# Kernel tuning notes

Measured on AMD Instinct MI355X. Metric: run time of the kernel, lower is better.

## Reference

```python
import jax, jax.numpy as jnp
import numpy as np

B, T, V, Dw, Df, H, L, F_ = 16, 96, 32000, 512, 512, 1024, 100, 64
EPS = 1e-8
SOS = 0


def setup_inputs() -> dict:
    key = jax.random.key(0)
    ks = jax.random.split(key, 24)
    rn = lambda k, s, sc=0.02: (jax.random.normal(k, s) * sc).astype(jnp.float32)
    pos_mask = (jax.random.uniform(ks[1], (B, F_, L)) < 0.3).astype(jnp.float32)
    pos_mask = jnp.maximum(pos_mask, jax.nn.one_hot(jnp.zeros((B, F_), jnp.int32), L))
    return {
        "fact_embeddings": rn(ks[0], (B, F_, Df), 1.0),
        "pos_mask": pos_mask,
        "emb": rn(ks[2], (V, Dw), 0.05),
        "W_ih": rn(ks[3], (4 * H, Df + Dw + L)),
        "W_hh": rn(ks[4], (4 * H, H)),
        "b_ih": jnp.zeros(4 * H, jnp.float32),
        "b_hh": jnp.zeros(4 * H, jnp.float32),
        "Wf1": rn(ks[5], (H, H + Df)), "bf1": jnp.zeros(H, jnp.float32),
        "Wf2": rn(ks[6], (Df, H)), "bf2": jnp.zeros(Df, jnp.float32),
        "Wc1": rn(ks[7], (H, H + Df)), "bc1": jnp.zeros(H, jnp.float32),
        "Wc2": rn(ks[8], (1, H)), "bc2": jnp.zeros(1, jnp.float32),
        "Wv1": rn(ks[9], (H, H + Df)), "bv1": jnp.zeros(H, jnp.float32),
        "Wv2": rn(ks[10], (Dw, H)), "bv2": jnp.zeros(Dw, jnp.float32),
        "Wp1": rn(ks[11], (H, H + Df)), "bp1": jnp.zeros(H, jnp.float32),
        "Wp2": rn(ks[12], (100, H)), "bp2": jnp.zeros(100, jnp.float32),
        "WP": rn(ks[13], (L, 100)), "bP": jnp.zeros(L, jnp.float32),
        "true_w": jax.random.randint(ks[14], (B, T), 0, L),
        "true_a": jax.random.randint(ks[15], (B, T), 0, F_),
        "true_z": jax.random.randint(ks[16], (B, T), 0, 2),
        "num_facts": jax.random.randint(ks[17], (B,), 1, F_),
    }


def reference(fact_embeddings, pos_mask, emb, W_ih, W_hh, b_ih, b_hh,
              Wf1, bf1, Wf2, bf2, Wc1, bc1, Wc2, bc2,
              Wv1, bv1, Wv2, bv2, Wp1, bp1, Wp2, bp2, WP, bP,
              true_w, true_a, true_z, num_facts):
    def mlp(x, W1, b1, W2, b2):
        return W2 @ jax.nn.relu(W1 @ x + b1) + b2

    def single(fe, pmask_b, tw, ta, tz, nf):
        # fe: [F_, Df]  pmask_b: [F_, L]  tw/ta/tz: [T]
        idx = jnp.arange(F_)
        valid = (idx < nf).astype(jnp.float32)
        attn_mask = jnp.where(idx == F_ - 1, 1.0, valid)  # NaF slot always allowed
        e_k = (fe * valid[:, None]).sum(0) / nf.astype(jnp.float32)

        def step(carry, inputs):
            a_prev, h, c, wv, wo = carry
            w_t, a_true, z_true = inputs
            x = jnp.concatenate([a_prev, wv, wo])  # [Df+Dw+L]
            gates = W_ih @ x + b_ih + W_hh @ h + b_hh
            i_g, f_g, g_g, o_g = jnp.split(gates, 4)
            c = jax.nn.sigmoid(f_g) * c + jax.nn.sigmoid(i_g) * jnp.tanh(g_g)
            h = jax.nn.sigmoid(o_g) * jnp.tanh(c)
            oe = jnp.concatenate([h, e_k])
            k_fact = mlp(oe, Wf1, bf1, Wf2, bf2)           # [Df]
            prob_a = jax.nn.softmax(fe @ k_fact)           # [F_]
            m = attn_mask * prob_a + EPS
            m = m / m.sum()
            log_m = jnp.log(m)
            a_idx = jnp.argmax(m)
            a_vec = fe[a_idx]
            oa = jnp.concatenate([h, a_vec])
            z = jax.nn.sigmoid(mlp(oa, Wc1, bc1, Wc2, bc2))[0]
            k_voca = mlp(oa, Wv1, bv1, Wv2, bv2)           # [Dw]
            log_w = jax.nn.log_softmax(emb @ k_voca)       # [V]
            k_pos = mlp(oa, Wp1, bp1, Wp2, bp2)            # [100]
            prob_pos = jax.nn.softmax(WP @ k_pos + bP)     # [L]
            mp = pmask_b[a_true] * prob_pos + EPS
            mp = mp / mp.sum()
            log_pos = jnp.log(mp)
            zf = z_true.astype(jnp.float32)
            loss = (-log_m[a_true]
                    + jnp.where(z_true == 0, -log_w[w_t], -log_pos[w_t])
                    - (zf * jnp.log(z) + (1.0 - zf) * jnp.log(1.0 - z)))
            wv_next = jnp.where(z_true == 0, emb[w_t], jnp.zeros(Dw, jnp.float32))
            wo_next = jnp.where(z_true == 0, jnp.zeros(L, jnp.float32), jax.nn.one_hot(w_t, L))
            return (a_vec, h, c, wv_next, wo_next), loss

        carry0 = (jnp.zeros(Df, jnp.float32), jnp.zeros(H, jnp.float32),
                  jnp.zeros(H, jnp.float32), emb[SOS], jnp.zeros(L, jnp.float32))
        _, losses = jax.lax.scan(step, carry0, (tw, ta, tz))
        return losses.sum()

    return jax.vmap(single)(fact_embeddings, pos_mask, true_w, true_a, true_z, num_facts).sum()
```

## Files before the change

### kernel.cpp

```cpp
#include <hip/hip_runtime.h>
#include <math.h>

#define TT 96
#define VV 32000
#define EPSF 1e-8f

typedef __attribute__((ext_vector_type(8))) short short8;
typedef __attribute__((ext_vector_type(4))) float f4v;

__device__ __forceinline__ float wsum64(float v){
  #pragma unroll
  for (int m=32;m>0;m>>=1) v += __shfl_xor(v,m);
  return v;
}
__device__ __forceinline__ float sigm(float x){ return 1.0f/(1.0f+expf(-x)); }
__device__ __forceinline__ float softplus(float x){ return x>20.0f ? x : log1pf(expf(x)); }
__device__ __forceinline__ float bf2f(unsigned short u){ return __uint_as_float(((unsigned)u)<<16); }
__device__ __forceinline__ unsigned short f2bf(float f){
  unsigned u = __float_as_uint(f);
  return (unsigned short)((u + 0x7fffu + ((u>>16)&1u)) >> 16);
}

__device__ __forceinline__ void st_dc(float* p, float v){
  __hip_atomic_store(p, v, __ATOMIC_RELAXED, __HIP_MEMORY_SCOPE_AGENT);
}
__device__ __forceinline__ void st_dc_i(int* p, int v){
  __hip_atomic_store(p, v, __ATOMIC_RELAXED, __HIP_MEMORY_SCOPE_AGENT);
}
__device__ __forceinline__ int ld_dc_i(const int* p){
  return __hip_atomic_load(p, __ATOMIC_RELAXED, __HIP_MEMORY_SCOPE_AGENT);
}
__device__ __forceinline__ unsigned ld_cnt(const unsigned* p){
  return __hip_atomic_load(p, __ATOMIC_RELAXED, __HIP_MEMORY_SCOPE_AGENT);
}
__device__ __forceinline__ float2 ld_dc_2(const float* p){
  union { unsigned long long u; float2 f; } cv;
  cv.u = __hip_atomic_load((const unsigned long long*)p, __ATOMIC_RELAXED, __HIP_MEMORY_SCOPE_AGENT);
  return cv.f;
}

__device__ __forceinline__ void bar_full(unsigned* cntA, unsigned* rel, unsigned epoch){
  __syncthreads();
  if (threadIdx.x == 0)
    __hip_atomic_fetch_add(cntA + (blockIdx.x & 7)*64, 1u, __ATOMIC_RELAXED, __HIP_MEMORY_SCOPE_AGENT);
  if (blockIdx.x == 0){
    if (threadIdx.x < 64){
      unsigned tgt = epoch * 32u;
      while (true){
        unsigned v = (threadIdx.x < 8) ? ld_cnt(cntA + threadIdx.x*64) : tgt;
        if (__all(v >= tgt)) break;
        __builtin_amdgcn_s_sleep(1);
      }
      if (threadIdx.x == 0)
        __hip_atomic_store(rel, epoch, __ATOMIC_RELAXED, __HIP_MEMORY_SCOPE_AGENT);
    }
  } else {
    if (threadIdx.x == 0){
      while (ld_cnt(rel) < epoch) __builtin_amdgcn_s_sleep(1);
    }
  }
  __syncthreads();
}

__device__ __forceinline__ void core_chunk(
  const float4* __restrict__ w0, const float4* __restrict__ w1,
  const float4* __restrict__ w2, const float4* __restrict__ w3,
  const float4* __restrict__ xl, int l, int g, float (&acc)[4][4])
{
  #pragma unroll
  for (int kt=0; kt<8; kt++){
    int i = kt*16 + l;
    float4 a0=w0[i], a1=w1[i], a2=w2[i], a3=w3[i];
    #pragma unroll
    for (int j=0;j<4;j++){
      float4 x = xl[(4*g+j)*129 + i];
      acc[0][j] += a0.x*x.x + a0.y*x.y + a0.z*x.z + a0.w*x.w;
      acc[1][j] += a1.x*x.x + a1.y*x.y + a1.z*x.z + a1.w*x.w;
      acc[2][j] += a2.x*x.x + a2.y*x.y + a2.z*x.z + a2.w*x.w;
      acc[3][j] += a3.x*x.x + a3.y*x.y + a3.z*x.z + a3.w*x.w;
    }
  }
}

__device__ __forceinline__ float reduce_pick(float (&acc)[4][4], int l){
  float r = 0.f;
  #pragma unroll
  for (int ri=0;ri<4;ri++)
  #pragma unroll
  for (int j=0;j<4;j++){
    float v = acc[ri][j];
    v += __shfl_xor(v,1); v += __shfl_xor(v,2);
    v += __shfl_xor(v,4); v += __shfl_xor(v,8);
    if (l == ri*4+j) r = v;
  }
  return r;
}

__global__ __launch_bounds__(256) void k_phase1(
  const float* __restrict__ Whh, float* __restrict__ hall,
  const float* __restrict__ Pw, const float* __restrict__ Pa,
  int* __restrict__ aall, float* __restrict__ c,
  const float* __restrict__ Wf1, const float* __restrict__ cf,
  float* __restrict__ tf,
  const float* __restrict__ Gb, const float* __restrict__ gb0,
  const int* __restrict__ ta, const int* __restrict__ nfp,
  float* __restrict__ loss,
  unsigned* __restrict__ cntA, unsigned* __restrict__ cntB,
  unsigned* __restrict__ rel)
{
  __shared__ float4 xl[16*129];
  __shared__ float sg[256];
  __shared__ float sS[64];
  __shared__ int   sai[16];
  int tid = threadIdx.x, lane = tid & 63, wave = tid >> 6;
  int l = lane & 15, g = lane >> 4;
  int wg = blockIdx.x;

  for (int t=0; t<TT; t++){
    {
      int j0 = wg*4;
      const float4* h4 = (const float4*)hall + (size_t)t*4096;
      float acc[4][4] = {};
      for (int kc=0; kc<2; kc++){
        for (int idx=tid; idx<2048; idx+=256){
          int b = idx>>7, i = idx&127;
          xl[b*129+i] = h4[b*256 + kc*128 + i];
        }
        __syncthreads();
        const float4* w0 = (const float4*)(Whh + (size_t)(wave*1024 + j0+0)*1024) + kc*128;
        const float4* w1 = (const float4*)(Whh + (size_t)(wave*1024 + j0+1)*1024) + kc*128;
        const float4* w2 = (const float4*)(Whh + (size_t)(wave*1024 + j0+2)*1024) + kc*128;
        const float4* w3 = (const float4*)(Whh + (size_t)(wave*1024 + j0+3)*1024) + kc*128;
        core_chunk(w0,w1,w2,w3, xl, l, g, acc);
        __syncthreads();
      }
      float v = reduce_pick(acc, l);
      if (t > 0 && tid < 64){
        bool need = (tid < 16);
        while (true){
          int vv = need ? ld_dc_i(&aall[(t-1)*64 + tid]) : 1;
          if (__all(vv != 0)){ if (need) sai[tid] = vv - 1; break; }
          __builtin_amdgcn_s_sleep(1);
        }
      }
      __syncthreads();
      int r = l>>2;
      int b = g*4 + (l&3);
      int row = wave*1024 + j0 + r;
      float e = __builtin_nontemporal_load(Pw + ((size_t)(b*96+t))*4096 + row);
      if (t > 0){
        int ai = sai[b];
        e += __builtin_nontemporal_load(Pa + ((size_t)(b*64+ai))*4096 + row);
      }
      sg[wave*64 + r*16 + b] = v + e;
      __syncthreads();
      if (tid < 64){
        int jj = j0 + (tid>>4), bb = tid&15;
        float ig = sg[  0 + (tid>>4)*16 + bb];
        float fg = sg[ 64 + (tid>>4)*16 + bb];
        float gg = sg[128 + (tid>>4)*16 + bb];
        float og = sg[192 + (tid>>4)*16 + bb];
        int ci = bb*1024 + jj;
        float cn = sigm(fg)*c[ci] + sigm(ig)*tanhf(gg);
        c[ci] = cn;
        st_dc(&hall[((size_t)(t+1)*16 + bb)*1024 + jj], sigm(og)*tanhf(cn));
      }
    }
    bar_full(cntA, rel, (unsigned)(t+1));

    if (wg < 64){
      int rl0 = wg*16 + wave*4;
      const float4* h4 = (const float4*)hall + (size_t)(t+1)*4096;
      float acc[4][4] = {};
      for (int kc=0; kc<2; kc++){
        for (int idx=tid; idx<2048; idx+=256){
          int b = idx>>7, i = idx&127;
          xl[b*129+i] = h4[b*256 + kc*128 + i];
        }
        __syncthreads();
        const float4* w0 = (const float4*)(Wf1 + (size_t)(rl0+0)*1536) + kc*128;
        const float4* w1 = (const float4*)(Wf1 + (size_t)(rl0+1)*1536) + kc*128;
        const float4* w2 = (const float4*)(Wf1 + (size_t)(rl0+2)*1536) + kc*128;
        const float4* w3 = (const float4*)(Wf1 + (size_t)(rl0+3)*1536) + kc*128;
        core_chunk(w0,w1,w2,w3, xl, l, g, acc);
        __syncthreads();
      }
      float v = reduce_pick(acc, l);
      int rl = rl0 + (l>>2);
      int b = g*4 + (l&3);
      float* tfb = tf + (t&1)*16384;
      st_dc(&tfb[b*1024 + rl], fmaxf(v + cf[b*1024 + rl], 0.f));
      __syncthreads();
      if (tid == 0)
        __hip_atomic_fetch_add(cntB + (wg&7)*64, 1u, __ATOMIC_RELAXED, __HIP_MEMORY_SCOPE_AGENT);
    }

    if (wg >= 240){
      int b = wg - 240;
      if (tid < 64){
        unsigned tgt = (unsigned)(t+1) * 8u;
        while (true){
          unsigned vv = (tid < 8) ? ld_cnt(cntB + tid*64) : tgt;
          if (__all(vv >= tgt)) break;
          __builtin_amdgcn_s_sleep(1);
        }
      }
      __syncthreads();
      const float* tfb = tf + (t&1)*16384;
      float* stf = (float*)xl;
      {
        const float* src = tfb + b*1024;
        float2 c0 = ld_dc_2(src + 4*tid + 0);
        float2 c1 = ld_dc_2(src + 4*tid + 2);
        ((float2*)stf)[2*tid+0] = c0;
        ((float2*)stf)[2*tid+1] = c1;
      }
      __syncthreads();
      int f = tid>>2, q = tid&3;
      const float4* G4 = (const float4*)(Gb + (size_t)(b*64+f)*1024);
      const float4* st4 = (const float4*)stf;
      float acc = 0.f;
      for (int j=0;j<64;j++){
        int i = q*64 + j;
        float4 a = G4[i], x = st4[i];
        acc += a.x*x.x + a.y*x.y + a.z*x.z + a.w*x.w;
      }
      acc += __shfl_xor(acc,1);
      acc += __shfl_xor(acc,2);
      if (q==0) sS[f] = acc + gb0[b*64+f];
      __syncthreads();
      if (tid < 64){
        int nf = nfp[b];
        float s = sS[tid];
        float mx = s;
        #pragma unroll
        for (int m=32;m>0;m>>=1) mx = fmaxf(mx, __shfl_xor(mx,m));
        float p = expf(s - mx);
        float ps = wsum64(p);
        p /= ps;
        bool mask = (tid < nf) || (tid == 63);
        float mval = mask ? (p + EPSF) : EPSF;
        float msum = wsum64(mval);
        float bv = mval; int bi2 = tid;
        #pragma unroll
        for (int m=32;m>0;m>>=1){
          float ov = __shfl_xor(bv,m); int oi = __shfl_xor(bi2,m);
          if (ov > bv || (ov == bv && oi < bi2)){ bv = ov; bi2 = oi; }
        }
        int at = ta[b*TT + t];
        float mat = __shfl(mval, at);
        if (tid == 0){
          atomicAdd(loss, -(logf(mat) - logf(msum)));
          st_dc_i(&aall[t*64 + b], bi2 + 1);
        }
      }
      __syncthreads();
    }
  }
}


__global__ __launch_bounds__(256) void k2_cvp(
  const float* __restrict__ Wc1, const float* __restrict__ Wv1,
  const float* __restrict__ Wp1, const float* __restrict__ hall,
  const float* __restrict__ Ph, const int* __restrict__ aall,
  const float* __restrict__ bc1, const float* __restrict__ bv1,
  const float* __restrict__ bp1, float* __restrict__ tcvp)
{
  __shared__ float4 xl[16*129];
  int tid = threadIdx.x, lane = tid & 63, wave = tid >> 6;
  int l = lane & 15, g = lane >> 4;
  int seg = blockIdx.x >> 6;
  int rl0 = (blockIdx.x & 63)*16 + wave*4;
  const float* W = (seg==0)?Wc1:(seg==1)?Wv1:Wp1;
  const float4* h4 = (const float4*)hall + (size_t)(16 + blockIdx.y*16)*256;
  float acc[4][4] = {};
  for (int kc=0; kc<2; kc++){
    for (int idx=tid; idx<2048; idx+=256){
      int cc = idx>>7, i = idx&127;
      xl[cc*129+i] = h4[cc*256 + kc*128 + i];
    }
    __syncthreads();
    const float4* w0 = (const float4*)(W + (size_t)(rl0+0)*1536) + kc*128;
    const float4* w1 = (const float4*)(W + (size_t)(rl0+1)*1536) + kc*128;
    const float4* w2 = (const float4*)(W + (size_t)(rl0+2)*1536) + kc*128;
    const float4* w3 = (const float4*)(W + (size_t)(rl0+3)*1536) + kc*128;
    core_chunk(w0,w1,w2,w3, xl, l, g, acc);
    __syncthreads();
  }
  float v = reduce_pick(acc, l);
  int rl = rl0 + (l>>2);
  int n = blockIdx.y*16 + g*4 + (l&3);
  int b = n & 15;
  int ai = aall[(n>>4)*64 + (n&15)] - 1;
  const float* bias = (seg==0)?bc1:(seg==1)?bv1:bp1;
  float vv = v + Ph[((size_t)(b*64+ai))*3072 + seg*1024 + rl] + bias[rl];
  tcvp[(size_t)n*3072 + seg*1024 + rl] = fmaxf(vv, 0.f);
}

__global__ __launch_bounds__(256) void k2_heads2(
  const float* __restrict__ Wv2, const float* __restrict__ bv2,
  const float* __restrict__ Wp2, const float* __restrict__ bp2,
  const float* __restrict__ Wc2, const float* __restrict__ bc2,
  const float* __restrict__ tcvp, unsigned short* __restrict__ kvh,
  float* __restrict__ kpall, float* __restrict__ zlall)
{
  __shared__ float4 xl[16*129];
  int tid = threadIdx.x, lane = tid & 63, wave = tid >> 6;
  int l = lane & 15, g = lane >> 4;
  int bx = blockIdx.x;
  int seg = (bx < 32) ? 0 : (bx < 39) ? 1 : 2;
  int rb  = (seg==0) ? bx*16 : (seg==1) ? (bx-32)*16 : 0;
  int rl0 = rb + wave*4;
  const float* WS = (seg==0)?Wv2:(seg==1)?Wp2:Wc2;
  int maxr = (seg==0)?511:(seg==1)?99:0;
  int xoff4 = (seg==0)?256:(seg==1)?512:0;
  const float4* X4 = (const float4*)tcvp;
  float acc[4][4] = {};
  for (int kc=0; kc<2; kc++){
    for (int idx=tid; idx<2048; idx+=256){
      int cc = idx>>7, i = idx&127;
      xl[cc*129+i] = X4[(size_t)(blockIdx.y*16+cc)*768 + xoff4 + kc*128 + i];
    }
    __syncthreads();
    const float4* w0 = (const float4*)(WS + (size_t)min(rl0+0,maxr)*1024) + kc*128;
    const float4* w1 = (const float4*)(WS + (size_t)min(rl0+1,maxr)*1024) + kc*128;
    const float4* w2 = (const float4*)(WS + (size_t)min(rl0+2,maxr)*1024) + kc*128;
    const float4* w3 = (const float4*)(WS + (size_t)min(rl0+3,maxr)*1024) + kc*128;
    core_chunk(w0,w1,w2,w3, xl, l, g, acc);
    __syncthreads();
  }
  float v = reduce_pick(acc, l);
  int rl = rl0 + (l>>2);
  int n = blockIdx.y*16 + g*4 + (l&3);
  if (seg==0) kvh[(size_t)n*512 + rl] = f2bf(v + bv2[rl]);
  else if (seg==1){ if (rl < 100) kpall[n*128 + rl] = v + bp2[rl]; }
  else { if (rl == 0) zlall[n] = v + bc2[0]; }
}

__global__ __launch_bounds__(256) void k2_vocab(
  const unsigned short* __restrict__ embh, const unsigned short* __restrict__ kvh,
  float2* __restrict__ part)
{
  int wid = blockIdx.x*4 + (threadIdx.x>>6);
  int lane = threadIdx.x & 63;
  int mtile = wid % 500, ntile = wid / 500;
  int mrow = mtile*64 + (lane&15);
  int ncol = ntile*64 + (lane&15);
  int ko = (lane>>4)*8;
  f4v acc[4][4];
  #pragma unroll
  for (int i=0;i<4;i++)
  #pragma unroll
  for (int j=0;j<4;j++)
  #pragma unroll
  for (int r=0;r<4;r++) acc[i][j][r] = 0.f;
  for (int kk=0; kk<512; kk+=32){
    short8 af[4], bfr[4];
    #pragma unroll
    for (int i=0;i<4;i++)
      af[i] = *(const short8*)(embh + (size_t)(mrow+16*i)*512 + kk + ko);
    #pragma unroll
    for (int i=0;i<4;i++)
      bfr[i] = *(const short8*)(kvh + (size_t)(ncol+16*i)*512 + kk + ko);
    #pragma unroll
    for (int i=0;i<4;i++)
      #pragma unroll
      for (int j=0;j<4;j++)
        acc[i][j] = __builtin_amdgcn_mfma_f32_16x16x32_bf16(af[i], bfr[j], acc[i][j], 0,0,0);
  }
  int q = lane>>4;
  #pragma unroll
  for (int j=0;j<4;j++){
    float mx = -3.4e38f;
    #pragma unroll
    for (int i=0;i<4;i++)
    #pragma unroll
    for (int r=0;r<4;r++) mx = fmaxf(mx, acc[i][j][r]);
    mx = fmaxf(mx, __shfl_xor(mx,16));
    mx = fmaxf(mx, __shfl_xor(mx,32));
    float s = 0.f;
    #pragma unroll
    for (int i=0;i<4;i++)
    #pragma unroll
    for (int r=0;r<4;r++) s += expf(acc[i][j][r] - mx);
    s += __shfl_xor(s,16);
    s += __shfl_xor(s,32);
    if (q==0){
      int col = ntile*64 + 16*j + (lane&15);
      part[(size_t)col*500 + mtile] = make_float2(mx, s);
    }
  }
}

__global__ __launch_bounds__(256) void k2_vfin(
  const float2* __restrict__ part, const unsigned short* __restrict__ embh,
  const unsigned short* __restrict__ kvh, const int* __restrict__ tw,
  const int* __restrict__ tz, float* __restrict__ loss)
{
  __shared__ float red[4];
  int n = blockIdx.x, tid = threadIdx.x;
  int t = n>>4, b = n&15;
  float mx = -3.4e38f;
  for (int i=tid; i<500; i+=256) mx = fmaxf(mx, part[(size_t)n*500+i].x);
  #pragma unroll
  for (int m=32;m>0;m>>=1) mx = fmaxf(mx, __shfl_xor(mx,m));
  if ((tid&63)==0) red[tid>>6] = mx;
  __syncthreads();
  float M = fmaxf(fmaxf(red[0],red[1]), fmaxf(red[2],red[3]));
  __syncthreads();
  float s = 0.f;
  for (int i=tid; i<500; i+=256){
    float2 p = part[(size_t)n*500+i];
    s += p.y * expf(p.x - M);
  }
  s = wsum64(s);
  if ((tid&63)==0) red[tid>>6] = s;
  __syncthreads();
  float S = red[0]+red[1]+red[2]+red[3];
  __syncthreads();
  int w = tw[b*96+t];
  float d = 0.f;
  {
    const unsigned short* er = embh + (size_t)w*512;
    const unsigned short* kr = kvh + (size_t)n*512;
    for (int i=tid; i<512; i+=256) d += bf2f(er[i])*bf2f(kr[i]);
  }
  d = wsum64(d);
  if ((tid&63)==0) red[tid>>6] = d;
  __syncthreads();
  if (tid==0 && tz[b*96+t]==0){
    float D = red[0]+red[1]+red[2]+red[3];
    atomicAdd(loss, -(D - (M + logf(S))));
  }
}

__global__ __launch_bounds__(128) void k2_posz(
  const float* __restrict__ kpall, const float* __restrict__ zlall,
  const float* __restrict__ WP, const float* __restrict__ bP,
  const float* __restrict__ pmask, const int* __restrict__ tw,
  const int* __restrict__ ta, const int* __restrict__ tz,
  float* __restrict__ loss)
{
  __shared__ float pp[100];
  int n = blockIdx.x, tid = threadIdx.x;
  int t = n>>4, b = n&15;
  if (tid < 100){
    float s = bP[tid];
    const float* wr = WP + tid*100;
    const float* kp = kpall + n*128;
    for (int j=0;j<100;j++) s += wr[j]*kp[j];
    pp[tid] = s;
  }
  __syncthreads();
  if (tid == 0){
    float u = zlall[n];
    int z = tz[b*96+t], w = tw[b*96+t], at = ta[b*96+t];
    float tot = z ? softplus(-u) : softplus(u);
    if (z){
      float mxv = -1e30f;
      for (int l2=0;l2<100;l2++) mxv = fmaxf(mxv, pp[l2]);
      float se = 0.f;
      for (int l2=0;l2<100;l2++) se += expf(pp[l2]-mxv);
      const float* pm = pmask + ((size_t)b*64 + at)*100;
      float msum = 0.f, mw = 0.f;
      for (int l2=0;l2<100;l2++){
        float m = pm[l2]*(expf(pp[l2]-mxv)/se) + EPSF;
        msum += m;
        if (l2==w) mw = m;
      }
      tot += -(logf(mw) - logf(msum));
    }
    atomicAdd(loss, tot);
  }
}


__global__ void k_cvt_emb(const float* __restrict__ emb, unsigned* __restrict__ out){
  const int n = VV*512/2;
  for (int idx = blockIdx.x*256 + threadIdx.x; idx < n; idx += gridDim.x*256){
    float2 v = ((const float2*)emb)[idx];
    unsigned a = __float_as_uint(v.x), b = __float_as_uint(v.y);
    unsigned ra = (a + 0x7fffu + ((a>>16)&1u)) >> 16;
    unsigned rb = (b + 0x7fffu + ((b>>16)&1u)) >> 16;
    out[idx] = ra | (rb<<16);
  }
}

__global__ void k_setup(const float* __restrict__ fe, const int* __restrict__ nfp,
                        float* __restrict__ e_k){
  int b = blockIdx.x, tid = threadIdx.x;
  int nf = nfp[b];
  for (int d=tid; d<512; d+=256){
    float s = 0.f;
    for (int f=0; f<nf; f++) s += fe[((size_t)b*64+f)*512 + d];
    e_k[b*512+d] = s/(float)nf;
  }
}

__global__ __launch_bounds__(256) void k_pre_pa(
  const float* __restrict__ Wih, const float* __restrict__ fe, float* __restrict__ Pa)
{
  __shared__ float4 xl[16*129];
  int tid = threadIdx.x, lane = tid & 63, wave = tid >> 6;
  int l = lane & 15, g = lane >> 4;
  int row0 = blockIdx.x*16 + wave*4;
  int c0 = blockIdx.y*16;
  const float4* fe4 = (const float4*)fe;
  for (int idx=tid; idx<2048; idx+=256){
    int cc = idx>>7, i = idx&127;
    xl[cc*129+i] = fe4[(size_t)(c0+cc)*128 + i];
  }
  __syncthreads();
  const float4* w0 = (const float4*)(Wih + (size_t)(row0+0)*1124);
  const float4* w1 = (const float4*)(Wih + (size_t)(row0+1)*1124);
  const float4* w2 = (const float4*)(Wih + (size_t)(row0+2)*1124);
  const float4* w3 = (const float4*)(Wih + (size_t)(row0+3)*1124);
  float acc[4][4] = {};
  core_chunk(w0,w1,w2,w3, xl, l, g, acc);
  float v = reduce_pick(acc, l);
  int row = row0 + (l>>2), c = c0 + g*4 + (l&3);
  Pa[(size_t)c*4096 + row] = v;
}

__global__ __launch_bounds__(256) void k_pre_ph(
  const float* __restrict__ Wc1, const float* __restrict__ Wv1,
  const float* __restrict__ Wp1, const float* __restrict__ fe, float* __restrict__ Ph)
{
  __shared__ float4 xl[16*129];
  int tid = threadIdx.x, lane = tid & 63, wave = tid >> 6;
  int l = lane & 15, g = lane >> 4;
  int row0 = blockIdx.x*16 + wave*4;
  int head = row0 >> 10, rl0 = row0 & 1023;
  const float* W = (head==0)?Wc1:(head==1)?Wv1:Wp1;
  int c0 = blockIdx.y*16;
  const float4* fe4 = (const float4*)fe;
  for (int idx=tid; idx<2048; idx+=256){
    int cc = idx>>7, i = idx&127;
    xl[cc*129+i] = fe4[(size_t)(c0+cc)*128 + i];
  }
  __syncthreads();
  const float4* w0 = (const float4*)(W + (size_t)(rl0+0)*1536 + 1024);
  const float4* w1 = (const float4*)(W + (size_t)(rl0+1)*1536 + 1024);
  const float4* w2 = (const float4*)(W + (size_t)(rl0+2)*1536 + 1024);
  const float4* w3 = (const float4*)(W + (size_t)(rl0+3)*1536 + 1024);
  float acc[4][4] = {};
  core_chunk(w0,w1,w2,w3, xl, l, g, acc);
  float v = reduce_pick(acc, l);
  int row = row0 + (l>>2), c = c0 + g*4 + (l&3);
  Ph[(size_t)c*3072 + row] = v;
}

__global__ __launch_bounds__(256) void k_pre_pw(
  const float* __restrict__ Wih, const float* __restrict__ emb,
  const int* __restrict__ tw, const int* __restrict__ tz,
  const float* __restrict__ bih, const float* __restrict__ bhh,
  float* __restrict__ Pw)
{
  __shared__ float4 xl[16*129];
  int tid = threadIdx.x, lane = tid & 63, wave = tid >> 6;
  int l = lane & 15, g = lane >> 4;
  int row0 = blockIdx.x*16 + wave*4;
  int c0 = blockIdx.y*16;
  for (int idx=tid; idx<2048; idx+=256){
    int cc = idx>>7, i = idx&127;
    int c = c0+cc, b = c/96, t2 = c - b*96;
    int w=0, z=0;
    if (t2>0){ w = tw[b*96+t2-1]; z = tz[b*96+t2-1]; }
    float4 v = make_float4(0.f,0.f,0.f,0.f);
    if (z==0) v = ((const float4*)emb)[(size_t)w*128 + i];
    xl[cc*129+i] = v;
  }
  __syncthreads();
  const float4* w0 = (const float4*)(Wih + (size_t)(row0+0)*1124 + 512);
  const float4* w1 = (const float4*)(Wih + (size_t)(row0+1)*1124 + 512);
  const float4* w2 = (const float4*)(Wih + (size_t)(row0+2)*1124 + 512);
  const float4* w3 = (const float4*)(Wih + (size_t)(row0+3)*1124 + 512);
  float acc[4][4] = {};
  core_chunk(w0,w1,w2,w3, xl, l, g, acc);
  float v = reduce_pick(acc, l);
  int row = row0 + (l>>2), c = c0 + g*4 + (l&3);
  int b = c/96, t2 = c - b*96;
  int w=0, z=0;
  if (t2>0){ w = tw[b*96+t2-1]; z = tz[b*96+t2-1]; }
  v += bih[row] + bhh[row];
  if (z) v += Wih[(size_t)row*1124 + 1024 + w];
  Pw[(size_t)c*4096 + row] = v;
}

__global__ __launch_bounds__(256) void k_pre_cf(
  const float* __restrict__ Wf1, const float* __restrict__ bf1,
  const float* __restrict__ e_k, float* __restrict__ cf)
{
  __shared__ float4 xl[16*129];
  int tid = threadIdx.x, lane = tid & 63, wave = tid >> 6;
  int l = lane & 15, g = lane >> 4;
  int row0 = blockIdx.x*16 + wave*4;
  const float4* ek4 = (const float4*)e_k;
  for (int idx=tid; idx<2048; idx+=256){
    int cc = idx>>7, i = idx&127;
    xl[cc*129+i] = ek4[cc*128 + i];
  }
  __syncthreads();
  const float4* w0 = (const float4*)(Wf1 + (size_t)(row0+0)*1536 + 1024);
  const float4* w1 = (const float4*)(Wf1 + (size_t)(row0+1)*1536 + 1024);
  const float4* w2 = (const float4*)(Wf1 + (size_t)(row0+2)*1536 + 1024);
  const float4* w3 = (const float4*)(Wf1 + (size_t)(row0+3)*1536 + 1024);
  float acc[4][4] = {};
  core_chunk(w0,w1,w2,w3, xl, l, g, acc);
  float v = reduce_pick(acc, l);
  int row = row0 + (l>>2), b = g*4 + (l&3);
  cf[b*1024 + row] = v + bf1[row];
}

__global__ __launch_bounds__(256) void k_pre_g(
  const float* __restrict__ Wf2, const float* __restrict__ fe, float* __restrict__ Gb)
{
  __shared__ float fs[16][128];
  int tid = threadIdx.x;
  int r0 = blockIdx.x*16;
  int k0 = blockIdx.y*256;
  float acc[16] = {};
  for (int dc=0; dc<4; dc++){
    for (int idx=tid; idx<2048; idx+=256){
      int r = idx>>7, d = idx&127;
      fs[r][d] = fe[(size_t)(r0+r)*512 + dc*128 + d];
    }
    __syncthreads();
    for (int d=0; d<128; d++){
      float w = Wf2[(size_t)(dc*128+d)*1024 + k0 + tid];
      #pragma unroll
      for (int r=0;r<16;r++) acc[r] += fs[r][d]*w;
    }
    __syncthreads();
  }
  #pragma unroll
  for (int r=0;r<16;r++) Gb[(size_t)(r0+r)*1024 + k0 + tid] = acc[r];
}

__global__ __launch_bounds__(256) void k_gb0(
  const float* __restrict__ fe, const float* __restrict__ bf2, float* __restrict__ gb0)
{
  int b = blockIdx.x;
  int f = threadIdx.x>>2, q = threadIdx.x&3;
  const float4* fe4 = (const float4*)(fe + ((size_t)b*64+f)*512);
  const float4* b4 = (const float4*)bf2;
  float acc = 0.f;
  for (int j=0;j<32;j++){
    int i = q*32+j;
    float4 a = fe4[i], x = b4[i];
    acc += a.x*x.x + a.y*x.y + a.z*x.z + a.w*x.w;
  }
  acc += __shfl_xor(acc,1);
  acc += __shfl_xor(acc,2);
  if (q==0) gb0[b*64+f] = acc;
}

__global__ void k_out(const float* __restrict__ loss, float* __restrict__ out){
  out[0] = loss[0];
}

extern "C" void kernel_launch(void* const* d_in, const int* in_sizes, int n_in,
                              void* d_out, int out_size, void* d_ws, size_t ws_size,
                              hipStream_t stream)
{
  const float* fe   = (const float*)d_in[0];
  const float* pmask= (const float*)d_in[1];
  const float* emb  = (const float*)d_in[2];
  const float* Wih  = (const float*)d_in[3];
  const float* Whh  = (const float*)d_in[4];
  const float* bih  = (const float*)d_in[5];
  const float* bhh  = (const float*)d_in[6];
  const float* Wf1  = (const float*)d_in[7];
  const float* bf1  = (const float*)d_in[8];
  const float* Wf2  = (const float*)d_in[9];
  const float* bf2  = (const float*)d_in[10];
  const float* Wc1  = (const float*)d_in[11];
  const float* bc1  = (const float*)d_in[12];
  const float* Wc2  = (const float*)d_in[13];
  const float* bc2  = (const float*)d_in[14];
  const float* Wv1  = (const float*)d_in[15];
  const float* bv1  = (const float*)d_in[16];
  const float* Wv2  = (const float*)d_in[17];
  const float* bv2  = (const float*)d_in[18];
  const float* Wp1  = (const float*)d_in[19];
  const float* bp1  = (const float*)d_in[20];
  const float* Wp2  = (const float*)d_in[21];
  const float* bp2  = (const float*)d_in[22];
  const float* WP   = (const float*)d_in[23];
  const float* bP   = (const float*)d_in[24];
  const int* tw  = (const int*)d_in[25];
  const int* ta  = (const int*)d_in[26];
  const int* tz  = (const int*)d_in[27];
  const int* nfp = (const int*)d_in[28];

  float* w = (float*)d_ws;
  float*    loss  = w + 0;
  unsigned* cntA  = (unsigned*)(w + 64);
  unsigned* cntB  = (unsigned*)(w + 576);
  unsigned* rel   = (unsigned*)(w + 1088);
  float*    c     = w + 2048;
  float*    hall  = w + 18432;
  int*      aall  = (int*)(w + 1607680);
  float*    tf    = w + 1613824;
  float*    gb0   = w + 1646592;
  float*    e_k   = w + 1647616;
  float*    cf    = w + 1655808;
  float*    kpall = w + 1672192;
  float*    zlall = w + 1868800;
  float*    tcvp  = w + 1870336;
  float*    Gb    = w + 1870336;
  float2*   part  = (float2*)(w + 6588928);
  unsigned short* kvh = (unsigned short*)(w + 8124928);
  float*    Pa    = w + 8518144;
  float*    Ph    = w + 12712448;
  float*    Pw    = w + 15858176;
  unsigned* embbf = (unsigned*)(w + 22149632);
  const unsigned short* embh = (const unsigned short*)embbf;

  hipMemsetAsync(d_ws, 0, (size_t)34816*4, stream);
  hipMemsetAsync((void*)aall, 0, (size_t)96*64*4, stream);
  k_cvt_emb<<<8192,256,0,stream>>>(emb, embbf);
  k_setup<<<16,256,0,stream>>>(fe, nfp, e_k);
  k_pre_pa<<<dim3(256,64),256,0,stream>>>(Wih, fe, Pa);
  k_pre_ph<<<dim3(192,64),256,0,stream>>>(Wc1, Wv1, Wp1, fe, Ph);
  k_pre_pw<<<dim3(256,96),256,0,stream>>>(Wih, emb, tw, tz, bih, bhh, Pw);
  k_pre_cf<<<64,256,0,stream>>>(Wf1, bf1, e_k, cf);
  k_pre_g<<<dim3(64,4),256,0,stream>>>(Wf2, fe, Gb);
  k_gb0<<<16,256,0,stream>>>(fe, bf2, gb0);

  k_phase1<<<256,256,0,stream>>>(Whh, hall, Pw, Pa, aall, c, Wf1, cf, tf,
                                 Gb, gb0, ta, nfp, loss, cntA, cntB, rel);

  k2_cvp<<<dim3(192,96),256,0,stream>>>(Wc1, Wv1, Wp1, hall, Ph, aall,
                                        bc1, bv1, bp1, tcvp);
  k2_heads2<<<dim3(40,96),256,0,stream>>>(Wv2, bv2, Wp2, bp2, Wc2, bc2,
                                          tcvp, kvh, kpall, zlall);
  k2_vocab<<<3000,256,0,stream>>>(embh, kvh, part);
  k2_vfin<<<1536,256,0,stream>>>(part, embh, kvh, tw, tz, loss);
  k2_posz<<<1536,128,0,stream>>>(kpall, zlall, WP, bP, pmask, tw, ta, tz, loss);
  k_out<<<1,1,0,stream>>>(loss, (float*)d_out);
}
```

Baseline: 4.630 ms.

## Replace centralized grid barrier with decentralized counter polling and replicated attention indices

Removes the two-level grid barrier, where block 0 gathered counters and released a flag. Each block now increments one of 16 spread counters and waits by polling all counters itself. The LSTM step waits only at its start, and the Wf1 stage waits separately. The Pw load is issued before the wait to hide its latency, and the attention-index array is replicated 8 times so polling blocks spread across cache lines. This cuts barrier latency per timestep in the sequential recurrence, at the cost of more polling traffic and a larger workspace layout.

```diff
diff --git a/kernel.cpp b/kernel.cpp
--- a/kernel.cpp
+++ b/kernel.cpp
@@ -37,29 +37,6 @@
   union { unsigned long long u; float2 f; } cv;
   cv.u = __hip_atomic_load((const unsigned long long*)p, __ATOMIC_RELAXED, __HIP_MEMORY_SCOPE_AGENT);
   return cv.f;
-}
-
-__device__ __forceinline__ void bar_full(unsigned* cntA, unsigned* rel, unsigned epoch){
-  __syncthreads();
-  if (threadIdx.x == 0)
-    __hip_atomic_fetch_add(cntA + (blockIdx.x & 7)*64, 1u, __ATOMIC_RELAXED, __HIP_MEMORY_SCOPE_AGENT);
-  if (blockIdx.x == 0){
-    if (threadIdx.x < 64){
-      unsigned tgt = epoch * 32u;
-      while (true){
-        unsigned v = (threadIdx.x < 8) ? ld_cnt(cntA + threadIdx.x*64) : tgt;
-        if (__all(v >= tgt)) break;
-        __builtin_amdgcn_s_sleep(1);
-      }
-      if (threadIdx.x == 0)
-        __hip_atomic_store(rel, epoch, __ATOMIC_RELAXED, __HIP_MEMORY_SCOPE_AGENT);
-    }
-  } else {
-    if (threadIdx.x == 0){
-      while (ld_cnt(rel) < epoch) __builtin_amdgcn_s_sleep(1);
-    }
-  }
-  __syncthreads();
 }
 
 __device__ __forceinline__ void core_chunk(
@@ -105,8 +82,7 @@
   const float* __restrict__ Gb, const float* __restrict__ gb0,
   const int* __restrict__ ta, const int* __restrict__ nfp,
   float* __restrict__ loss,
-  unsigned* __restrict__ cntA, unsigned* __restrict__ cntB,
-  unsigned* __restrict__ rel)
+  unsigned* __restrict__ cntA, unsigned* __restrict__ cntB)
 {
   __shared__ float4 xl[16*129];
   __shared__ float sg[256];
@@ -119,12 +95,25 @@
   for (int t=0; t<TT; t++){
     {
       int j0 = wg*4;
+      int r = l>>2;
+      int b = g*4 + (l&3);
+      int row = wave*1024 + j0 + r;
+      float pwv = __builtin_nontemporal_load(Pw + ((size_t)(b*96+t))*4096 + row);
+      if (t > 0 && tid < 64){
+        unsigned tgt = (unsigned)t * 16u;
+        while (true){
+          unsigned v = (tid < 16) ? ld_cnt(cntA + tid*64) : tgt;
+          if (__all(v >= tgt)) break;
+          __builtin_amdgcn_s_sleep(1);
+        }
+      }
+      __syncthreads();
       const float4* h4 = (const float4*)hall + (size_t)t*4096;
       float acc[4][4] = {};
       for (int kc=0; kc<2; kc++){
         for (int idx=tid; idx<2048; idx+=256){
-          int b = idx>>7, i = idx&127;
-          xl[b*129+i] = h4[b*256 + kc*128 + i];
+          int bb = idx>>7, i = idx&127;
+          xl[bb*129+i] = h4[bb*256 + kc*128 + i];
         }
         __syncthreads();
         const float4* w0 = (const float4*)(Whh + (size_t)(wave*1024 + j0+0)*1024) + kc*128;
@@ -136,18 +125,16 @@
       }
       float v = reduce_pick(acc, l);
       if (t > 0 && tid < 64){
+        const int* ap = &aall[(t-1)*512 + (wg&7)*64];
         bool need = (tid < 16);
         while (true){
-          int vv = need ? ld_dc_i(&aall[(t-1)*64 + tid]) : 1;
+          int vv = need ? ld_dc_i(ap + tid) : 1;
           if (__all(vv != 0)){ if (need) sai[tid] = vv - 1; break; }
           __builtin_amdgcn_s_sleep(1);
         }
       }
       __syncthreads();
-      int r = l>>2;
-      int b = g*4 + (l&3);
-      int row = wave*1024 + j0 + r;
-      float e = __builtin_nontemporal_load(Pw + ((size_t)(b*96+t))*4096 + row);
+      float e = pwv;
       if (t > 0){
         int ai = sai[b];
         e += __builtin_nontemporal_load(Pa + ((size_t)(b*64+ai))*4096 + row);
@@ -165,17 +152,28 @@
         c[ci] = cn;
         st_dc(&hall[((size_t)(t+1)*16 + bb)*1024 + jj], sigm(og)*tanhf(cn));
       }
-    }
-    bar_full(cntA, rel, (unsigned)(t+1));
+      __syncthreads();
+      if (tid == 0)
+        __hip_atomic_fetch_add(cntA + (wg&15)*64, 1u, __ATOMIC_RELAXED, __HIP_MEMORY_SCOPE_AGENT);
+    }
 
     if (wg < 64){
+      if (tid < 64){
+        unsigned tgt = (unsigned)(t+1) * 16u;
+        while (true){
+          unsigned v = (tid < 16) ? ld_cnt(cntA + tid*64) : tgt;
+          if (__all(v >= tgt)) break;
+          __builtin_amdgcn_s_sleep(1);
+        }
+      }
+      __syncthreads();
       int rl0 = wg*16 + wave*4;
       const float4* h4 = (const float4*)hall + (size_t)(t+1)*4096;
       float acc[4][4] = {};
       for (int kc=0; kc<2; kc++){
         for (int idx=tid; idx<2048; idx+=256){
-          int b = idx>>7, i = idx&127;
-          xl[b*129+i] = h4[b*256 + kc*128 + i];
+          int bb = idx>>7, i = idx&127;
+          xl[bb*129+i] = h4[bb*256 + kc*128 + i];
         }
         __syncthreads();
         const float4* w0 = (const float4*)(Wf1 + (size_t)(rl0+0)*1536) + kc*128;
@@ -251,7 +249,9 @@
         float mat = __shfl(mval, at);
         if (tid == 0){
           atomicAdd(loss, -(logf(mat) - logf(msum)));
-          st_dc_i(&aall[t*64 + b], bi2 + 1);
+          #pragma unroll
+          for (int gg2=0; gg2<8; gg2++)
+            st_dc_i(&aall[t*512 + gg2*64 + b], bi2 + 1);
         }
       }
       __syncthreads();
@@ -292,7 +292,7 @@
   int rl = rl0 + (l>>2);
   int n = blockIdx.y*16 + g*4 + (l&3);
   int b = n & 15;
-  int ai = aall[(n>>4)*64 + (n&15)] - 1;
+  int ai = aall[(n>>4)*512 + (n&15)] - 1;
   const float* bias = (seg==0)?bc1:(seg==1)?bv1:bp1;
   float vv = v + Ph[((size_t)(b*64+ai))*3072 + seg*1024 + rl] + bias[rl];
   tcvp[(size_t)n*3072 + seg*1024 + rl] = fmaxf(vv, 0.f);
@@ -697,29 +697,28 @@
   float* w = (float*)d_ws;
   float*    loss  = w + 0;
   unsigned* cntA  = (unsigned*)(w + 64);
-  unsigned* cntB  = (unsigned*)(w + 576);
-  unsigned* rel   = (unsigned*)(w + 1088);
+  unsigned* cntB  = (unsigned*)(w + 1088);
   float*    c     = w + 2048;
   float*    hall  = w + 18432;
   int*      aall  = (int*)(w + 1607680);
-  float*    tf    = w + 1613824;
-  float*    gb0   = w + 1646592;
-  float*    e_k   = w + 1647616;
-  float*    cf    = w + 1655808;
-  float*    kpall = w + 1672192;
-  float*    zlall = w + 1868800;
-  float*    tcvp  = w + 1870336;
-  float*    Gb    = w + 1870336;
-  float2*   part  = (float2*)(w + 6588928);
-  unsigned short* kvh = (unsigned short*)(w + 8124928);
-  float*    Pa    = w + 8518144;
-  float*    Ph    = w + 12712448;
-  float*    Pw    = w + 15858176;
-  unsigned* embbf = (unsigned*)(w + 22149632);
+  float*    tf    = w + 1656832;
+  float*    gb0   = w + 1689600;
+  float*    e_k   = w + 1690624;
+  float*    cf    = w + 1698816;
+  float*    kpall = w + 1715200;
+  float*    zlall = w + 1911808;
+  float*    tcvp  = w + 1913344;
+  float*    Gb    = w + 1913344;
+  float2*   part  = (float2*)(w + 6631936);
+  unsigned short* kvh = (unsigned short*)(w + 8167936);
+  float*    Pa    = w + 8561152;
+  float*    Ph    = w + 12755456;
+  float*    Pw    = w + 15901184;
+  unsigned* embbf = (unsigned*)(w + 22192640);
   const unsigned short* embh = (const unsigned short*)embbf;
 
   hipMemsetAsync(d_ws, 0, (size_t)34816*4, stream);
-  hipMemsetAsync((void*)aall, 0, (size_t)96*64*4, stream);
+  hipMemsetAsync((void*)aall, 0, (size_t)96*512*4, stream);
   k_cvt_emb<<<8192,256,0,stream>>>(emb, embbf);
   k_setup<<<16,256,0,stream>>>(fe, nfp, e_k);
   k_pre_pa<<<dim3(256,64),256,0,stream>>>(Wih, fe, Pa);
@@ -730,7 +729,7 @@
   k_gb0<<<16,256,0,stream>>>(fe, bf2, gb0);
 
   k_phase1<<<256,256,0,stream>>>(Whh, hall, Pw, Pa, aall, c, Wf1, cf, tf,
-                                 Gb, gb0, ta, nfp, loss, cntA, cntB, rel);
+                                 Gb, gb0, ta, nfp, loss, cntA, cntB);
 
   k2_cvp<<<dim3(192,96),256,0,stream>>>(Wc1, Wv1, Wp1, hall, Ph, aall,
                                         bc1, bv1, bp1, tcvp);
```

Result: no change. 4.637 ms (+0.1%).
